# Performance work log

Measured on AMD Instinct MI355X. Metric: run time of the kernel, lower is better.

The kernel has to match this reference:

```python
import jax, jax.numpy as jnp
import numpy as np

HEAD_DIM = 64


def rotate_half(x):
    x1, x2 = jnp.split(x, 2, axis=-1)
    return jnp.concatenate((-x2, x1), axis=-1)


def setup_inputs() -> dict:
    key = jax.random.key(0)
    ks = jax.random.split(key, 12)
    B, S, H, Hkv, D, hid = 1, 1536, 64, 8, HEAD_DIM, 2880
    std = 0.02
    x = jax.random.normal(ks[0], (B, S, hid), jnp.float32)
    # real RoPE cache, layout [cos | sin] of shape (S, 2*D)
    inv = 1.0 / (10000.0 ** (np.arange(0, D, 2, dtype=np.float32) / D))
    freqs = np.outer(np.arange(S, dtype=np.float32), inv)          # (S, D/2)
    emb = np.concatenate([freqs, freqs], axis=-1)                  # (S, D)
    rope_cache = jnp.asarray(
        np.concatenate([np.cos(emb), np.sin(emb)], axis=-1), jnp.float32
    )
    return {
        "x": x,
        "rope_cache": rope_cache,
        "wq_w": jax.random.normal(ks[1], (H * D, hid), jnp.float32) * std,
        "wq_b": jax.random.normal(ks[2], (H * D,), jnp.float32) * std,
        "wk_w": jax.random.normal(ks[3], (Hkv * D, hid), jnp.float32) * std,
        "wk_b": jax.random.normal(ks[4], (Hkv * D,), jnp.float32) * std,
        "wv_w": jax.random.normal(ks[5], (Hkv * D, hid), jnp.float32) * std,
        "wv_b": jax.random.normal(ks[6], (Hkv * D,), jnp.float32) * std,
        "wo_w": jax.random.normal(ks[7], (hid, H * D), jnp.float32) * std,
        "wo_b": jax.random.normal(ks[8], (hid,), jnp.float32) * std,
        "sinks": jax.random.normal(ks[9], (H,), jnp.float32) * std,
    }


def reference(x, rope_cache, wq_w, wq_b, wk_w, wk_b, wv_w, wv_b, wo_w, wo_b, sinks):
    B, S, hid = x.shape
    D = HEAD_DIM
    H = wq_w.shape[0] // D
    Hkv = wk_w.shape[0] // D
    n_rep = H // Hkv

    q = (x @ wq_w.T + wq_b).reshape(B, S, H, D)
    k = (x @ wk_w.T + wk_b).reshape(B, S, Hkv, D)
    v = (x @ wv_w.T + wv_b).reshape(B, S, Hkv, D)

    # RoPE (rotate-half form); rope_cache[:, :D]=cos, [:, D:]=sin
    cos = rope_cache[:S, :D][None, :, None, :]
    sin = rope_cache[:S, D:][None, :, None, :]
    q = q * cos + rotate_half(q) * sin
    k = k * cos + rotate_half(k) * sin

    # GQA repeat_kv: interleaved repeat along head dim
    k = jnp.repeat(k, n_rep, axis=2)  # (B, S, H, D)
    v = jnp.repeat(v, n_rep, axis=2)

    scale = 1.0 / jnp.sqrt(jnp.asarray(D, x.dtype))
    scores = jnp.einsum("bqhd,bkhd->bhqk", q, k) * scale  # (B, H, S, S)
    i = jnp.arange(S)
    causal = i[:, None] >= i[None, :]
    neg = jnp.asarray(jnp.finfo(scores.dtype).min, scores.dtype)
    scores = jnp.where(causal[None, None], scores, neg)

    lse = jax.nn.logsumexp(scores, axis=-1)               # (B, H, S)
    attn = jax.nn.softmax(scores, axis=-1)
    out = jnp.einsum("bhqk,bkhd->bqhd", attn, v)          # (B, S, H, D)

    # attention-sink rescale: sigmoid(lse - sink_logit)
    sink_scale = jax.nn.sigmoid(lse - sinks[None, :, None])  # (B, H, S)
    out = out * jnp.transpose(sink_scale, (0, 2, 1))[..., None]

    out = out.reshape(B, S, H * D)
    return out @ wo_w.T + wo_b
```

## Files before the change

kernel.cpp:

```cpp
#include <hip/hip_runtime.h>

typedef unsigned short u16;
typedef unsigned int u32;
typedef __attribute__((ext_vector_type(8))) __bf16 bf16x8;
typedef __attribute__((ext_vector_type(8))) u16 u16x8;
typedef __attribute__((ext_vector_type(4))) u16 u16x4;
typedef __attribute__((ext_vector_type(4))) float f32x4;
typedef __attribute__((ext_vector_type(2))) u32 u32x2;

#define DEV static __device__ __forceinline__

DEV u16 f2bf(float f) {
  unsigned u = __builtin_bit_cast(unsigned, f);
  u += 0x7FFFu + ((u >> 16) & 1u);
  return (u16)(u >> 16);
}

DEV float ex2(float x) { return __builtin_amdgcn_exp2f(x); }

DEV u32 cvt_pk_bf16(float lo, float hi) {
  u32 r;
  asm("v_cvt_pk_bf16_f32 %0, %1, %2" : "=v"(r) : "v"(lo), "v"(hi));
  return r;
}

DEV f32x4 mfma16(bf16x8 a, bf16x8 b, f32x4 c) {
  return __builtin_amdgcn_mfma_f32_16x16x32_bf16(a, b, c, 0, 0, 0);
}

DEV f32x4 fmax4(f32x4 a, f32x4 b) {
  f32x4 r;
  r[0] = fmaxf(a[0], b[0]); r[1] = fmaxf(a[1], b[1]);
  r[2] = fmaxf(a[2], b[2]); r[3] = fmaxf(a[3], b[3]);
  return r;
}

DEV void gload_lds16(const u16* g, u16* lds) {
  __builtin_amdgcn_global_load_lds(
      (const __attribute__((address_space(1))) void*)g,
      (__attribute__((address_space(3))) void*)lds, 16, 0, 0);
}

DEV void vm_wait6() { asm volatile("s_waitcnt vmcnt(6)" ::: "memory"); }
DEV void vm_wait2() { asm volatile("s_waitcnt vmcnt(2)" ::: "memory"); }
DEV void vm_wait0() { asm volatile("s_waitcnt vmcnt(0)" ::: "memory"); }

__global__ __launch_bounds__(256) void cvt_all(
    const float* __restrict__ x, const float* __restrict__ wq,
    const float* __restrict__ wk, const float* __restrict__ wv,
    const float* __restrict__ wo, const float* __restrict__ qb,
    const float* __restrict__ kb, const float* __restrict__ vb,
    u16* __restrict__ x_bf, u16* __restrict__ wqkv_bf,
    u16* __restrict__ wo_bf, float* __restrict__ bias_p) {
  const int NX = 1536 * 2880 / 4;
  const int NWQ = 4096 * 2880 / 4;
  const int NWKV = 512 * 2880 / 4;
  const int NWO = 2944 * 4096 / 4;
  const int C0 = NX, C1 = C0 + NWQ, C2 = C1 + NWKV, C3 = C2 + NWKV;
  const int C4 = C3 + NWO, C5 = C4 + 5120 / 4;
  int i = blockIdx.x * 256 + threadIdx.x;
  if (i >= C5) return;
  if (i < C4) {
    const float* s;
    u16* d;
    bool pad = false;
    if (i < C0) { s = x + (size_t)i * 4; d = x_bf + (size_t)i * 4; }
    else if (i < C1) { size_t q = i - C0; s = wq + q * 4; d = wqkv_bf + q * 4; }
    else if (i < C2) { size_t q = i - C1; s = wk + q * 4; d = wqkv_bf + (size_t)NWQ * 4 + q * 4; }
    else if (i < C3) { size_t q = i - C2; s = wv + q * 4; d = wqkv_bf + (size_t)(NWQ + NWKV) * 4 + q * 4; }
    else {
      size_t q = i - C3;
      int row = (int)(q >> 10);
      pad = (row >= 2880);
      s = wo + q * 4; d = wo_bf + q * 4;
    }
    u16x4 o;
    if (!pad) {
      float4 v = *(const float4*)s;
      o = (u16x4){f2bf(v.x), f2bf(v.y), f2bf(v.z), f2bf(v.w)};
    } else {
      o = (u16x4){0, 0, 0, 0};
    }
    *(u16x4*)d = o;
  } else {
    int e = (i - C4) * 4;
#pragma unroll
    for (int j = 0; j < 4; j++) {
      int idx = e + j;
      bias_p[idx] = (idx < 4096) ? qb[idx] : (idx < 4608 ? kb[idx - 4096] : vb[idx - 4608]);
    }
  }
}

__global__ __launch_bounds__(256) void gemm_bt64(const u16* __restrict__ A,
                                                 const u16* __restrict__ B,
                                                 const float* __restrict__ bias,
                                                 float* __restrict__ C,
                                                 int M, int K, int Nreal, int ldc) {
  __shared__ u16 smA[2][128 * 64];
  __shared__ u16 smB[2][64 * 64];
  int nbm = M >> 7;
  int chunk = gridDim.x >> 3;
  int wg = (blockIdx.x & 7) * chunk + (blockIdx.x >> 3);
  int bm = wg % nbm, bn = wg / nbm;
  int t = threadIdx.x, lane = t & 63;
  int wv = t >> 6;
  int l15 = lane & 15, hi = lane >> 4;
  f32x4 acc[2][4] = {};
  int tr = t >> 3;
  int scol = ((t & 7) ^ (tr & 7)) * 8;
  const u16* Ab = A + (size_t)(bm * 128 + tr) * K + scol;
  const u16* Bb = B + (size_t)(bn * 64 + tr) * K + scol;

  auto stage = [&](int b, int ks) {
    int k0 = ks * 64;
#pragma unroll
    for (int i = 0; i < 4; i++)
      gload_lds16(Ab + k0 + (size_t)i * 32 * K, &smA[b][i * 2048 + t * 8]);
#pragma unroll
    for (int i = 0; i < 2; i++)
      gload_lds16(Bb + k0 + (size_t)i * 32 * K, &smB[b][i * 2048 + t * 8]);
  };

  int NK = K >> 6;
  stage(0, 0);
  if (NK > 1) stage(1, 1);
  for (int ks = 0; ks < NK; ks++) {
    int cur = ks & 1;
    if (ks + 1 < NK) vm_wait6(); else vm_wait0();
    __builtin_amdgcn_s_barrier();
    __builtin_amdgcn_sched_barrier(0);
#pragma unroll
    for (int kk = 0; kk < 2; kk++) {
      int sc = ((kk * 4 + hi) ^ (l15 & 7)) * 8;
      bf16x8 af[2], bfr[4];
#pragma unroll
      for (int m = 0; m < 2; m++)
        af[m] = *(const bf16x8*)(&smA[cur][(wv * 32 + m * 16 + l15) * 64 + sc]);
#pragma unroll
      for (int n = 0; n < 4; n++)
        bfr[n] = *(const bf16x8*)(&smB[cur][(n * 16 + l15) * 64 + sc]);
      __builtin_amdgcn_s_setprio(1);
#pragma unroll
      for (int m = 0; m < 2; m++)
#pragma unroll
        for (int n = 0; n < 4; n++)
          acc[m][n] = mfma16(af[m], bfr[n], acc[m][n]);
      __builtin_amdgcn_s_setprio(0);
    }
    __builtin_amdgcn_s_barrier();
    if (ks + 2 < NK) stage(cur, ks + 2);
  }
  int r0 = bm * 128 + wv * 32 + hi * 4;
  int c0 = bn * 64 + l15;
#pragma unroll
  for (int n = 0; n < 4; n++) {
    int col = c0 + n * 16;
    if (col >= Nreal) continue;
    float bv = bias[col];
#pragma unroll
    for (int m = 0; m < 2; m++) {
#pragma unroll
      for (int r = 0; r < 4; r++) {
        C[(size_t)(r0 + m * 16 + r) * ldc + col] = acc[m][n][r] + bv;
      }
    }
  }
}

__global__ __launch_bounds__(256) void rope_tr(const float* __restrict__ src,
                                               const float* __restrict__ rope,
                                               u16* __restrict__ dst,
                                               int S, int H, int ld, int col0,
                                               float scale) {
  int i = blockIdx.x * 256 + threadIdx.x;
  if (i >= S * H * 64) return;
  int d = i & 63;
  int s = (i >> 6) % S;
  int h = i / (S * 64);
  const float* base = src + (size_t)s * ld + col0 + h * 64;
  float q = base[d];
  float qp = base[(d + 32) & 63];
  float c = rope[s * 128 + d];
  float sn = rope[s * 128 + 64 + d];
  float r = (d < 32) ? (q * c - qp * sn) : (q * c + qp * sn);
  dst[i] = f2bf(r * scale);
}

__global__ __launch_bounds__(256) void cast_trT(const float* __restrict__ src,
                                                u16* __restrict__ dst, int S, int Hkv,
                                                int ld, int col0) {
  __shared__ u16 tile[64][65];
  int s0 = blockIdx.x * 64;
  int hkv = blockIdx.y;
  int t = threadIdx.x;
  int dl = (t & 15) * 4;
  int sl = t >> 4;
#pragma unroll
  for (int j = 0; j < 4; j++) {
    int s = sl + j * 16;
    float4 v = *(const float4*)(src + (size_t)(s0 + s) * ld + col0 + hkv * 64 + dl);
    tile[dl + 0][s] = f2bf(v.x);
    tile[dl + 1][s] = f2bf(v.y);
    tile[dl + 2][s] = f2bf(v.z);
    tile[dl + 3][s] = f2bf(v.w);
  }
  __syncthreads();
  int sl2 = (t & 7) * 8;
  int dl2 = t >> 3;
#pragma unroll
  for (int j = 0; j < 2; j++) {
    int d = dl2 + j * 32;
    u16x8 o;
#pragma unroll
    for (int c = 0; c < 8; c++) o[c] = tile[d][sl2 + c];
    *(u16x8*)(dst + ((size_t)hkv * 64 + d) * S + s0 + sl2) = o;
  }
}

__global__ __launch_bounds__(512) void attn_fwd(const u16* __restrict__ Q,
                                                const u16* __restrict__ K,
                                                const u16* __restrict__ VT,
                                                const float* __restrict__ sinks,
                                                u16* __restrict__ Out,
                                                int S, int H, int Hkv) {
  __shared__ u16 ldsK[2][64 * 64];
  __shared__ u16 ldsV[2][64 * 64];
  __shared__ u16 ldsP[8][16 * 64];
  int qb = gridDim.x - 1 - blockIdx.x;
  int h = blockIdx.y;
  int hkv = h / (H / Hkv);
  int t = threadIdx.x, lane = t & 63, wv = t >> 6;
  int l15 = lane & 15, hi = lane >> 4;
  int q0 = qb * 128 + wv * 16;
  const u16* Qh = Q + ((size_t)h * S + q0) * 64;
  const u16* Kh = K + (size_t)hkv * S * 64;
  const u16* VTh = VT + (size_t)hkv * 64 * S;
  u16* ldsPw = &ldsP[wv][0];
  int psw = (l15 & 7) << 4;

  bf16x8 qf[2];
  qf[0] = *(const bf16x8*)(Qh + l15 * 64 + hi * 8);
  qf[1] = *(const bf16x8*)(Qh + l15 * 64 + 32 + hi * 8);

  float mx = -1e30f, ls = 0.f;
  f32x4 ao[4] = {};

  auto stage = [&](int b, int kb) {
    int k0 = kb * 64;
    int row = t >> 3, c16 = t & 7;
    int sc = (c16 ^ (row & 7)) * 8;
    gload_lds16(Kh + (size_t)(k0 + row) * 64 + sc, &ldsK[b][t * 8]);
    gload_lds16(VTh + (size_t)row * S + k0 + sc, &ldsV[b][t * 8]);
  };

  int rowq = q0 + l15;
  int nkb = 2 * qb + 2;
  stage(0, 0);
  stage(1, 1);
  for (int kb = 0; kb < nkb; kb++) {
    int cur = kb & 1;
    if (kb + 1 < nkb) vm_wait2(); else vm_wait0();
    __builtin_amdgcn_s_barrier();
    __builtin_amdgcn_sched_barrier(0);
    if (kb * 64 <= q0 + 15) {
      f32x4 s[4] = {};
      __builtin_amdgcn_s_setprio(1);
#pragma unroll
      for (int kk = 0; kk < 2; kk++) {
#pragma unroll
        for (int ct = 0; ct < 4; ct++) {
          int row = ct * 16 + l15;
          int c16 = (kk * 4 + hi) ^ (row & 7);
          bf16x8 kf = *(const bf16x8*)(&ldsK[cur][row * 64 + c16 * 8]);
          s[ct] = mfma16(kf, qf[kk], s[ct]);
        }
      }
      __builtin_amdgcn_s_setprio(0);

      bool full = (kb * 64 + 63) < q0;
      if (!full) {
        int kc = kb * 64 + hi * 4;
#pragma unroll
        for (int ct = 0; ct < 4; ct++)
#pragma unroll
          for (int r = 0; r < 4; r++)
            if (kc + ct * 16 + r > rowq) s[ct][r] = -1e30f;
      }

      f32x4 mm = fmax4(fmax4(s[0], s[1]), fmax4(s[2], s[3]));
      float tmx = fmaxf(fmaxf(mm[0], mm[1]), fmaxf(mm[2], mm[3]));
      tmx = fmaxf(tmx, __shfl_xor(tmx, 16));
      tmx = fmaxf(tmx, __shfl_xor(tmx, 32));
      bool upd = __any(tmx > mx + 8.0f);
      if (upd) {
        float mn = fmaxf(mx, tmx);
        float al = ex2(mx - mn);
        mx = mn;
        ls *= al;
        float alr[4];
#pragma unroll
        for (int r = 0; r < 4; r++) alr[r] = __shfl(al, hi * 4 + r);
#pragma unroll
        for (int nt = 0; nt < 4; nt++)
#pragma unroll
          for (int r = 0; r < 4; r++) ao[nt][r] *= alr[r];
      }
#pragma unroll
      for (int ct = 0; ct < 4; ct++)
#pragma unroll
        for (int r = 0; r < 4; r++) s[ct][r] = ex2(s[ct][r] - mx);
      f32x4 sm = s[0] + s[1] + s[2] + s[3];
      float rs = (sm[0] + sm[1]) + (sm[2] + sm[3]);
      rs += __shfl_xor(rs, 16);
      rs += __shfl_xor(rs, 32);
      ls += rs;

#pragma unroll
      for (int ct = 0; ct < 4; ct++) {
        u32x2 pk = {cvt_pk_bf16(s[ct][0], s[ct][1]), cvt_pk_bf16(s[ct][2], s[ct][3])};
        *(u32x2*)(&ldsPw[(l15 * 128 + ((ct * 32 + hi * 8) ^ psw)) >> 1]) = pk;
      }

      __builtin_amdgcn_s_setprio(1);
#pragma unroll
      for (int kk = 0; kk < 2; kk++) {
        bf16x8 pa = *(const bf16x8*)(&ldsPw[(l15 * 128 + ((kk * 64 + hi * 16) ^ psw)) >> 1]);
#pragma unroll
        for (int nt = 0; nt < 4; nt++) {
          int vrow = nt * 16 + l15;
          int c16 = (kk * 4 + hi) ^ (vrow & 7);
          bf16x8 vf = *(const bf16x8*)(&ldsV[cur][vrow * 64 + c16 * 8]);
          ao[nt] = mfma16(pa, vf, ao[nt]);
        }
      }
      __builtin_amdgcn_s_setprio(0);
    }
    __builtin_amdgcn_s_barrier();
    if (kb + 2 < nkb) stage(cur, kb + 2);
  }

  float snk = sinks[h];
  float lse = 0.69314718056f * mx + __logf(ls);
  float ss = 1.f / (1.f + __expf(snk - lse));
  float f = ss / ls;
  float fr[4];
#pragma unroll
  for (int r = 0; r < 4; r++) fr[r] = __shfl(f, hi * 4 + r);
#pragma unroll
  for (int r = 0; r < 4; r++) {
    int row = q0 + hi * 4 + r;
#pragma unroll
    for (int nt = 0; nt < 4; nt++)
      Out[(size_t)row * (H * 64) + h * 64 + nt * 16 + l15] = f2bf(ao[nt][r] * fr[r]);
  }
}

extern "C" void kernel_launch(void* const* d_in, const int* in_sizes, int n_in,
                              void* d_out, int out_size, void* d_ws, size_t ws_size,
                              hipStream_t stream) {
  const int S = 1536, HID = 2880, H = 64, HKV = 8;
  const int NQ = 4096, NKV = 512, NQKV = 5120, NPAD = 2944;

  const float* x     = (const float*)d_in[0];
  const float* rope  = (const float*)d_in[1];
  const float* wq_w  = (const float*)d_in[2];
  const float* wq_b  = (const float*)d_in[3];
  const float* wk_w  = (const float*)d_in[4];
  const float* wk_b  = (const float*)d_in[5];
  const float* wv_w  = (const float*)d_in[6];
  const float* wv_b  = (const float*)d_in[7];
  const float* wo_w  = (const float*)d_in[8];
  const float* wo_b  = (const float*)d_in[9];
  const float* sinks = (const float*)d_in[10];
  float* out = (float*)d_out;

  char* ws = (char*)d_ws;
  size_t off = 0;
  auto alloc = [&](size_t bytes) {
    char* p = ws + off;
    off = (off + bytes + 255) & ~(size_t)255;
    return p;
  };
  u16*   x_bf    = (u16*)  alloc((size_t)S * HID * 2);
  u16*   wqkv_bf = (u16*)  alloc((size_t)NQKV * HID * 2);
  u16*   wo_bf   = (u16*)  alloc((size_t)NPAD * NQ * 2);
  float* qkv_raw = (float*)alloc((size_t)S * NQKV * 4);
  float* bias_p  = (float*)alloc((size_t)NQKV * 4);
  u16*   Qb      = (u16*)  alloc((size_t)H * S * 64 * 2);
  u16*   Kb      = (u16*)  alloc((size_t)HKV * S * 64 * 2);
  u16*   VTb     = (u16*)  alloc((size_t)HKV * 64 * S * 2);
  u16*   att     = (u16*)  alloc((size_t)S * NQ * 2);
  (void)ws_size; (void)n_in; (void)in_sizes; (void)out_size;

  auto cdiv = [](int a, int b) { return (a + b - 1) / b; };

  const int NCVT = S * HID / 4 + NQ * HID / 4 + 2 * (NKV * HID / 4) +
                   NPAD * NQ / 4 + NQKV / 4;
  cvt_all<<<cdiv(NCVT, 256), 256, 0, stream>>>(x, wq_w, wk_w, wv_w, wo_w,
                                               wq_b, wk_b, wv_b,
                                               x_bf, wqkv_bf, wo_bf, bias_p);

  gemm_bt64<<<(S / 128) * (NQKV / 64), 256, 0, stream>>>(x_bf, wqkv_bf, bias_p,
                                                         qkv_raw, S, HID, NQKV, NQKV);

  rope_tr<<<cdiv(S * NQ, 256), 256, 0, stream>>>(qkv_raw, rope, Qb, S, H, NQKV, 0,
                                                 0.125f * 1.44269504f);
  rope_tr<<<cdiv(S * NKV, 256), 256, 0, stream>>>(qkv_raw, rope, Kb, S, HKV, NQKV, NQ, 1.0f);
  cast_trT<<<dim3(S / 64, HKV), 256, 0, stream>>>(qkv_raw, VTb, S, HKV, NQKV, NQ + NKV);

  attn_fwd<<<dim3(S / 128, H), 512, 0, stream>>>(Qb, Kb, VTb, sinks, att, S, H, HKV);

  gemm_bt64<<<(S / 128) * (NPAD / 64), 256, 0, stream>>>(att, wo_bf, wo_b, out,
                                                         S, NQ, HID, HID);
}
```

Before: 224.1 us.

## Fuse RoPE and bf16 cast into QKV GEMM epilogue, enlarge GEMM tiles to 128x128

The QKV GEMM now applies bias, RoPE and the Q scale in its epilogue and writes bf16 directly into a packed QKV buffer. This removes the fp32 intermediate and the separate rope kernels. Attention reads Q and K straight from that packed layout using a 5120 stride. Both GEMMs switch to 128x128 tiles with 512 threads, and the output projection weight is padded to 3072 rows. The trade-off is more work per block and strided Q/K loads in attention.

```diff
diff --git a/kernel.cpp b/kernel.cpp
--- a/kernel.cpp
+++ b/kernel.cpp
@@ -41,7 +41,7 @@
       (__attribute__((address_space(3))) void*)lds, 16, 0, 0);
 }
 
-DEV void vm_wait6() { asm volatile("s_waitcnt vmcnt(6)" ::: "memory"); }
+DEV void vm_wait4() { asm volatile("s_waitcnt vmcnt(4)" ::: "memory"); }
 DEV void vm_wait2() { asm volatile("s_waitcnt vmcnt(2)" ::: "memory"); }
 DEV void vm_wait0() { asm volatile("s_waitcnt vmcnt(0)" ::: "memory"); }
 
@@ -55,7 +55,7 @@
   const int NX = 1536 * 2880 / 4;
   const int NWQ = 4096 * 2880 / 4;
   const int NWKV = 512 * 2880 / 4;
-  const int NWO = 2944 * 4096 / 4;
+  const int NWO = 3072 * 4096 / 4;
   const int C0 = NX, C1 = C0 + NWQ, C2 = C1 + NWKV, C3 = C2 + NWKV;
   const int C4 = C3 + NWO, C5 = C4 + 5120 / 4;
   int i = blockIdx.x * 256 + threadIdx.x;
@@ -92,42 +92,43 @@
   }
 }
 
-__global__ __launch_bounds__(256) void gemm_bt64(const u16* __restrict__ A,
-                                                 const u16* __restrict__ B,
-                                                 const float* __restrict__ bias,
-                                                 float* __restrict__ C,
-                                                 int M, int K, int Nreal, int ldc) {
+template <int MODE>
+__global__ __launch_bounds__(512) void gemm128(const u16* __restrict__ A,
+                                               const u16* __restrict__ B,
+                                               const float* __restrict__ bias,
+                                               float* __restrict__ C,
+                                               u16* __restrict__ Obf,
+                                               const float* __restrict__ rope,
+                                               int M, int K, int Nreal, int ldc) {
   __shared__ u16 smA[2][128 * 64];
-  __shared__ u16 smB[2][64 * 64];
+  __shared__ u16 smB[2][128 * 64];
   int nbm = M >> 7;
   int chunk = gridDim.x >> 3;
   int wg = (blockIdx.x & 7) * chunk + (blockIdx.x >> 3);
   int bm = wg % nbm, bn = wg / nbm;
-  int t = threadIdx.x, lane = t & 63;
-  int wv = t >> 6;
+  int t = threadIdx.x, lane = t & 63, wv = t >> 6;
+  int wr = wv >> 1, wc = wv & 1;
   int l15 = lane & 15, hi = lane >> 4;
   f32x4 acc[2][4] = {};
   int tr = t >> 3;
   int scol = ((t & 7) ^ (tr & 7)) * 8;
   const u16* Ab = A + (size_t)(bm * 128 + tr) * K + scol;
-  const u16* Bb = B + (size_t)(bn * 64 + tr) * K + scol;
+  const u16* Bb = B + (size_t)(bn * 128 + tr) * K + scol;
 
   auto stage = [&](int b, int ks) {
     int k0 = ks * 64;
-#pragma unroll
-    for (int i = 0; i < 4; i++)
-      gload_lds16(Ab + k0 + (size_t)i * 32 * K, &smA[b][i * 2048 + t * 8]);
-#pragma unroll
-    for (int i = 0; i < 2; i++)
-      gload_lds16(Bb + k0 + (size_t)i * 32 * K, &smB[b][i * 2048 + t * 8]);
+    gload_lds16(Ab + k0, &smA[b][t * 8]);
+    gload_lds16(Ab + k0 + (size_t)64 * K, &smA[b][4096 + t * 8]);
+    gload_lds16(Bb + k0, &smB[b][t * 8]);
+    gload_lds16(Bb + k0 + (size_t)64 * K, &smB[b][4096 + t * 8]);
   };
 
   int NK = K >> 6;
   stage(0, 0);
-  if (NK > 1) stage(1, 1);
+  stage(1, 1);
   for (int ks = 0; ks < NK; ks++) {
     int cur = ks & 1;
-    if (ks + 1 < NK) vm_wait6(); else vm_wait0();
+    if (ks + 1 < NK) vm_wait4(); else vm_wait0();
     __builtin_amdgcn_s_barrier();
     __builtin_amdgcn_sched_barrier(0);
 #pragma unroll
@@ -136,10 +137,10 @@
       bf16x8 af[2], bfr[4];
 #pragma unroll
       for (int m = 0; m < 2; m++)
-        af[m] = *(const bf16x8*)(&smA[cur][(wv * 32 + m * 16 + l15) * 64 + sc]);
+        af[m] = *(const bf16x8*)(&smA[cur][(wr * 32 + m * 16 + l15) * 64 + sc]);
 #pragma unroll
       for (int n = 0; n < 4; n++)
-        bfr[n] = *(const bf16x8*)(&smB[cur][(n * 16 + l15) * 64 + sc]);
+        bfr[n] = *(const bf16x8*)(&smB[cur][(wc * 64 + n * 16 + l15) * 64 + sc]);
       __builtin_amdgcn_s_setprio(1);
 #pragma unroll
       for (int m = 0; m < 2; m++)
@@ -151,43 +152,61 @@
     __builtin_amdgcn_s_barrier();
     if (ks + 2 < NK) stage(cur, ks + 2);
   }
-  int r0 = bm * 128 + wv * 32 + hi * 4;
-  int c0 = bn * 64 + l15;
-#pragma unroll
-  for (int n = 0; n < 4; n++) {
-    int col = c0 + n * 16;
-    if (col >= Nreal) continue;
-    float bv = bias[col];
-#pragma unroll
-    for (int m = 0; m < 2; m++) {
-#pragma unroll
-      for (int r = 0; r < 4; r++) {
-        C[(size_t)(r0 + m * 16 + r) * ldc + col] = acc[m][n][r] + bv;
-      }
-    }
-  }
-}
-
-__global__ __launch_bounds__(256) void rope_tr(const float* __restrict__ src,
-                                               const float* __restrict__ rope,
-                                               u16* __restrict__ dst,
-                                               int S, int H, int ld, int col0,
-                                               float scale) {
-  int i = blockIdx.x * 256 + threadIdx.x;
-  if (i >= S * H * 64) return;
-  int d = i & 63;
-  int s = (i >> 6) % S;
-  int h = i / (S * 64);
-  const float* base = src + (size_t)s * ld + col0 + h * 64;
-  float q = base[d];
-  float qp = base[(d + 32) & 63];
-  float c = rope[s * 128 + d];
-  float sn = rope[s * 128 + 64 + d];
-  float r = (d < 32) ? (q * c - qp * sn) : (q * c + qp * sn);
-  dst[i] = f2bf(r * scale);
-}
-
-__global__ __launch_bounds__(256) void cast_trT(const float* __restrict__ src,
+
+  int r0 = bm * 128 + wr * 32 + hi * 4;
+  int c0 = bn * 128 + wc * 64 + l15;
+  if (MODE == 0) {
+#pragma unroll
+    for (int n = 0; n < 4; n++) {
+      int col = c0 + n * 16;
+      if (col >= Nreal) continue;
+      float bv = bias[col];
+#pragma unroll
+      for (int m = 0; m < 2; m++)
+#pragma unroll
+        for (int r = 0; r < 4; r++)
+          C[(size_t)(r0 + m * 16 + r) * ldc + col] = acc[m][n][r] + bv;
+    }
+  } else {
+    float bv[4];
+#pragma unroll
+    for (int n = 0; n < 4; n++) bv[n] = bias[c0 + n * 16];
+    if (bn < 36) {
+      float scale = (bn < 32) ? 0.180336880f : 1.0f;
+#pragma unroll
+      for (int m = 0; m < 2; m++) {
+#pragma unroll
+        for (int r = 0; r < 4; r++) {
+          int s = r0 + m * 16 + r;
+          const float* rp = rope + (size_t)s * 128;
+          float cv0 = rp[l15], cv1 = rp[l15 + 16];
+          float sv0 = rp[64 + l15], sv1 = rp[64 + l15 + 16];
+          float v0 = acc[0][0][r], v1 = acc[0][1][r];
+          float v2 = acc[0][2][r], v3 = acc[0][3][r];
+          if (m) { v0 = acc[1][0][r]; v1 = acc[1][1][r]; v2 = acc[1][2][r]; v3 = acc[1][3][r]; }
+          v0 += bv[0]; v1 += bv[1]; v2 += bv[2]; v3 += bv[3];
+          u16* po = Obf + (size_t)s * 5120 + c0;
+          po[0]  = f2bf((v0 * cv0 - v2 * sv0) * scale);
+          po[16] = f2bf((v1 * cv1 - v3 * sv1) * scale);
+          po[32] = f2bf((v2 * cv0 + v0 * sv0) * scale);
+          po[48] = f2bf((v3 * cv1 + v1 * sv1) * scale);
+        }
+      }
+    } else {
+#pragma unroll
+      for (int m = 0; m < 2; m++)
+#pragma unroll
+        for (int r = 0; r < 4; r++) {
+          int s = r0 + m * 16 + r;
+          u16* po = Obf + (size_t)s * 5120 + c0;
+#pragma unroll
+          for (int n = 0; n < 4; n++) po[n * 16] = f2bf(acc[m][n][r] + bv[n]);
+        }
+    }
+  }
+}
+
+__global__ __launch_bounds__(256) void cast_trT(const u16* __restrict__ src,
                                                 u16* __restrict__ dst, int S, int Hkv,
                                                 int ld, int col0) {
   __shared__ u16 tile[64][65];
@@ -199,11 +218,11 @@
 #pragma unroll
   for (int j = 0; j < 4; j++) {
     int s = sl + j * 16;
-    float4 v = *(const float4*)(src + (size_t)(s0 + s) * ld + col0 + hkv * 64 + dl);
-    tile[dl + 0][s] = f2bf(v.x);
-    tile[dl + 1][s] = f2bf(v.y);
-    tile[dl + 2][s] = f2bf(v.z);
-    tile[dl + 3][s] = f2bf(v.w);
+    u16x4 v = *(const u16x4*)(src + (size_t)(s0 + s) * ld + col0 + hkv * 64 + dl);
+    tile[dl + 0][s] = v[0];
+    tile[dl + 1][s] = v[1];
+    tile[dl + 2][s] = v[2];
+    tile[dl + 3][s] = v[3];
   }
   __syncthreads();
   int sl2 = (t & 7) * 8;
@@ -218,8 +237,7 @@
   }
 }
 
-__global__ __launch_bounds__(512) void attn_fwd(const u16* __restrict__ Q,
-                                                const u16* __restrict__ K,
+__global__ __launch_bounds__(512) void attn_fwd(const u16* __restrict__ QKV,
                                                 const u16* __restrict__ VT,
                                                 const float* __restrict__ sinks,
                                                 u16* __restrict__ Out,
@@ -233,15 +251,15 @@
   int t = threadIdx.x, lane = t & 63, wv = t >> 6;
   int l15 = lane & 15, hi = lane >> 4;
   int q0 = qb * 128 + wv * 16;
-  const u16* Qh = Q + ((size_t)h * S + q0) * 64;
-  const u16* Kh = K + (size_t)hkv * S * 64;
+  const u16* Qh = QKV + (size_t)q0 * 5120 + h * 64;
+  const u16* Kh = QKV + 4096 + hkv * 64;
   const u16* VTh = VT + (size_t)hkv * 64 * S;
   u16* ldsPw = &ldsP[wv][0];
   int psw = (l15 & 7) << 4;
 
   bf16x8 qf[2];
-  qf[0] = *(const bf16x8*)(Qh + l15 * 64 + hi * 8);
-  qf[1] = *(const bf16x8*)(Qh + l15 * 64 + 32 + hi * 8);
+  qf[0] = *(const bf16x8*)(Qh + (size_t)l15 * 5120 + hi * 8);
+  qf[1] = *(const bf16x8*)(Qh + (size_t)l15 * 5120 + 32 + hi * 8);
 
   float mx = -1e30f, ls = 0.f;
   f32x4 ao[4] = {};
@@ -250,7 +268,7 @@
     int k0 = kb * 64;
     int row = t >> 3, c16 = t & 7;
     int sc = (c16 ^ (row & 7)) * 8;
-    gload_lds16(Kh + (size_t)(k0 + row) * 64 + sc, &ldsK[b][t * 8]);
+    gload_lds16(Kh + (size_t)(k0 + row) * 5120 + sc, &ldsK[b][t * 8]);
     gload_lds16(VTh + (size_t)row * S + k0 + sc, &ldsV[b][t * 8]);
   };
 
@@ -360,7 +378,7 @@
                               void* d_out, int out_size, void* d_ws, size_t ws_size,
                               hipStream_t stream) {
   const int S = 1536, HID = 2880, H = 64, HKV = 8;
-  const int NQ = 4096, NKV = 512, NQKV = 5120, NPAD = 2944;
+  const int NQ = 4096, NKV = 512, NQKV = 5120, NPAD = 3072;
 
   const float* x     = (const float*)d_in[0];
   const float* rope  = (const float*)d_in[1];
@@ -385,10 +403,8 @@
   u16*   x_bf    = (u16*)  alloc((size_t)S * HID * 2);
   u16*   wqkv_bf = (u16*)  alloc((size_t)NQKV * HID * 2);
   u16*   wo_bf   = (u16*)  alloc((size_t)NPAD * NQ * 2);
-  float* qkv_raw = (float*)alloc((size_t)S * NQKV * 4);
+  u16*   qkv_bf  = (u16*)  alloc((size_t)S * NQKV * 2);
   float* bias_p  = (float*)alloc((size_t)NQKV * 4);
-  u16*   Qb      = (u16*)  alloc((size_t)H * S * 64 * 2);
-  u16*   Kb      = (u16*)  alloc((size_t)HKV * S * 64 * 2);
   u16*   VTb     = (u16*)  alloc((size_t)HKV * 64 * S * 2);
   u16*   att     = (u16*)  alloc((size_t)S * NQ * 2);
   (void)ws_size; (void)n_in; (void)in_sizes; (void)out_size;
@@ -401,16 +417,13 @@
                                                wq_b, wk_b, wv_b,
                                                x_bf, wqkv_bf, wo_bf, bias_p);
 
-  gemm_bt64<<<(S / 128) * (NQKV / 64), 256, 0, stream>>>(x_bf, wqkv_bf, bias_p,
-                                                         qkv_raw, S, HID, NQKV, NQKV);
-
-  rope_tr<<<cdiv(S * NQ, 256), 256, 0, stream>>>(qkv_raw, rope, Qb, S, H, NQKV, 0,
-                                                 0.125f * 1.44269504f);
-  rope_tr<<<cdiv(S * NKV, 256), 256, 0, stream>>>(qkv_raw, rope, Kb, S, HKV, NQKV, NQ, 1.0f);
-  cast_trT<<<dim3(S / 64, HKV), 256, 0, stream>>>(qkv_raw, VTb, S, HKV, NQKV, NQ + NKV);
-
-  attn_fwd<<<dim3(S / 128, H), 512, 0, stream>>>(Qb, Kb, VTb, sinks, att, S, H, HKV);
-
-  gemm_bt64<<<(S / 128) * (NPAD / 64), 256, 0, stream>>>(att, wo_bf, wo_b, out,
-                                                         S, NQ, HID, HID);
-}
+  gemm128<1><<<(S / 128) * (NQKV / 128), 512, 0, stream>>>(
+      x_bf, wqkv_bf, bias_p, nullptr, qkv_bf, rope, S, HID, NQKV, NQKV);
+
+  cast_trT<<<dim3(S / 64, HKV), 256, 0, stream>>>(qkv_bf, VTb, S, HKV, NQKV, NQ + NKV);
+
+  attn_fwd<<<dim3(S / 128, H), 512, 0, stream>>>(qkv_bf, VTb, sinks, att, S, H, HKV);
+
+  gemm128<0><<<(S / 128) * (NPAD / 128), 512, 0, stream>>>(
+      att, wo_bf, wo_b, out, nullptr, nullptr, S, NQ, HID, HID);
+}
```

Measured after the change: 203.1 us. 1.1x faster.
